# Kernel tuning notes

Measured on AMD Instinct MI355X. Metric: run time of the kernel, lower is better.

## Reference

```python
import jax, jax.numpy as jnp
import numpy as np

N_NODES = 100000


def gcn_conv(x, edge_index, W, b):
    """PyG-style GCNConv: x' = D^-1/2 (A+I) D^-1/2 (x W) + b (self-loops added)."""
    n = x.shape[0]
    h = x @ W  # [N, out]
    loop = jnp.arange(n, dtype=edge_index.dtype)
    src = jnp.concatenate([edge_index[0], loop])  # [E+N]
    dst = jnp.concatenate([edge_index[1], loop])
    deg = jax.ops.segment_sum(jnp.ones_like(dst, dtype=h.dtype), dst, num_segments=n)
    dinv = jnp.where(deg > 0, jax.lax.rsqrt(deg), 0.0)
    norm = dinv[src] * dinv[dst]  # [E+N]
    # gather -> scale -> scatter-add aggregation
    out = jax.ops.segment_sum(norm[:, None] * h[src], dst, num_segments=n)
    return out + b


def setup_inputs() -> dict:
    key = jax.random.key(0)
    k1, k2, k3, k4 = jax.random.split(key, 4)
    n, e = N_NODES, 2560000
    x = jax.random.normal(k1, (n, 2), dtype=jnp.float32)
    edge_index = jax.random.randint(k2, (2, e), 0, n, dtype=jnp.int32)
    hidden = 32
    W1 = jax.random.normal(k3, (2, hidden), dtype=jnp.float32) * (1.0 / np.sqrt(2))
    b1 = jnp.zeros((hidden,), dtype=jnp.float32)
    W2 = jax.random.normal(k4, (hidden, 1), dtype=jnp.float32) * (1.0 / np.sqrt(hidden))
    b2 = jnp.zeros((1,), dtype=jnp.float32)
    return {"x": x, "edge_index": edge_index, "W1": W1, "b1": b1, "W2": W2, "b2": b2}


def reference(x, edge_index, W1, b1, W2, b2):
    h = jax.nn.relu(gcn_conv(x, edge_index, W1, b1))
    return gcn_conv(h, edge_index, W2, b2)  # [N, 1]
```

## Files before the change

### kernel.cpp

```cpp
#include <hip/hip_runtime.h>


#define NRMAX 32
#define AGG_BLKS 16
#define CHUNK 4096
#define NCHMAX 1024
#define DBITS 12
#define DMASK 4095


__global__ void k_px(const float2* __restrict__ x, const int* __restrict__ pdeg,
                     float* __restrict__ dinv, float2* __restrict__ px, int n) {
    int i = blockIdx.x * blockDim.x + threadIdx.x;
    if (i >= n) return;
    int deg = 1;
#pragma unroll
    for (int b = 0; b < AGG_BLKS; ++b) deg += pdeg[b * n + i];
    float d = rsqrtf((float)deg);
    dinv[i] = d;
    float2 xv = x[i];
    px[i] = make_float2(d * xv.x, d * xv.y);
}

__global__ void k_node(const float2* __restrict__ px, const float2* __restrict__ pP,
                       const float* __restrict__ dinv,
                       const float* __restrict__ W1, const float* __restrict__ b1,
                       const float* __restrict__ W2, float* __restrict__ s, int n) {
    int i = blockIdx.x * blockDim.x + threadIdx.x;
    if (i >= n) return;
    float2 v = px[i];
    float ax = v.x, ay = v.y;
#pragma unroll
    for (int b = 0; b < AGG_BLKS; ++b) {
        float2 p = pP[b * n + i];
        ax += p.x; ay += p.y;
    }
    float d = dinv[i];
    float dot = 0.f;
#pragma unroll
    for (int j = 0; j < 32; ++j) {
        float acc = fmaf(ax, W1[j], ay * W1[32 + j]);
        float h = fmaxf(fmaf(d, acc, b1[j]), 0.f);
        dot = fmaf(h, W2[j], dot);
    }
    s[i] = d * dot;
}

__global__ void k_out(const float* __restrict__ s, const float* __restrict__ ps,
                      const float* __restrict__ dinv, const float* __restrict__ b2,
                      float* __restrict__ out, int n) {
    int i = blockIdx.x * blockDim.x + threadIdx.x;
    if (i >= n) return;
    float acc = s[i];
#pragma unroll
    for (int b = 0; b < AGG_BLKS; ++b) acc += ps[b * n + i];
    out[i] = dinv[i] * acc + b2[0];
}


__global__ void k_cnt(const int* __restrict__ dst, int* __restrict__ cnt,
                      int e, int NR) {
    __shared__ int h[NRMAX];
    if (threadIdx.x < NRMAX) h[threadIdx.x] = 0;
    __syncthreads();
    int c0 = blockIdx.x * CHUNK;
    int c1 = min(c0 + CHUNK, e);
    int len = c1 - c0, lq = len >> 2;
    const int4* d4 = (const int4*)(dst + c0);
    for (int j = threadIdx.x; j < lq; j += blockDim.x) {
        int4 v = d4[j];
        atomicAdd(&h[v.x >> DBITS], 1);
        atomicAdd(&h[v.y >> DBITS], 1);
        atomicAdd(&h[v.z >> DBITS], 1);
        atomicAdd(&h[v.w >> DBITS], 1);
    }
    if (threadIdx.x == 0)
        for (int i = lq * 4; i < len; ++i) atomicAdd(&h[dst[c0 + i] >> DBITS], 1);
    __syncthreads();
    if (threadIdx.x < NR) cnt[(threadIdx.x << 10) + blockIdx.x] = h[threadIdx.x];
}

__global__ __launch_bounds__(1024)
void k_scan(const int* __restrict__ cnt, int* __restrict__ ofs,
            int* __restrict__ bstart, int* __restrict__ bcnt, int NR, int NCH) {
    __shared__ int tot[NRMAX], bs[NRMAX];
    int tid = threadIdx.x, lane = tid & 63, wid = tid >> 6;
    for (int r = wid; r < NR; r += 16) {
        int base = 0;
        for (int c0 = 0; c0 < NCH; c0 += 64) {
            int c = c0 + lane;
            int orig = (c < NCH) ? cnt[(r << 10) + c] : 0;
            int v = orig;
#pragma unroll
            for (int d = 1; d < 64; d <<= 1) {
                int u = __shfl_up(v, d);
                if (lane >= d) v += u;
            }
            if (c < NCH) ofs[(r << 10) + c] = base + v - orig;
            base += __shfl(v, 63);
        }
        tot[r] = base;
    }
    __syncthreads();
    if (tid == 0) {
        int acc = 0;
        for (int r = 0; r < NR; ++r) {
            bs[r] = acc; bstart[r] = acc; bcnt[r] = tot[r];
            acc += (tot[r] + 3) & ~3;
        }
    }
    __syncthreads();
    for (int i = tid; i < (NR << 10); i += 1024) {
        int c = i & (NCHMAX - 1);
        if (c < NCH) ofs[i] += bs[i >> 10];
    }
}

__global__ void k_bscatter(const int* __restrict__ src, const int* __restrict__ dst,
                           const int* __restrict__ ofs, unsigned* __restrict__ packed,
                           int e, int NR) {
    __shared__ int h[NRMAX], lofs[NRMAX], cur[NRMAX], gbase[NRMAX];
    __shared__ unsigned sbuf[CHUNK];
    int blk = blockIdx.x;
    int c0 = blk * CHUNK;
    int c1 = min(c0 + CHUNK, e);
    int len = c1 - c0, lq = len >> 2;
    if (threadIdx.x < NRMAX) h[threadIdx.x] = 0;
    __syncthreads();
    const int4* d4 = (const int4*)(dst + c0);
    const int4* s4 = (const int4*)(src + c0);
    for (int j = threadIdx.x; j < lq; j += blockDim.x) {
        int4 v = d4[j];
        atomicAdd(&h[v.x >> DBITS], 1);
        atomicAdd(&h[v.y >> DBITS], 1);
        atomicAdd(&h[v.z >> DBITS], 1);
        atomicAdd(&h[v.w >> DBITS], 1);
    }
    if (threadIdx.x == 0)
        for (int i = lq * 4; i < len; ++i) atomicAdd(&h[dst[c0 + i] >> DBITS], 1);
    __syncthreads();
    if (threadIdx.x == 0) {
        int acc = 0;
        for (int r = 0; r < NR; ++r) { lofs[r] = acc; acc += h[r]; }
    }
    __syncthreads();
    if (threadIdx.x < NR) {
        cur[threadIdx.x]   = lofs[threadIdx.x];
        gbase[threadIdx.x] = ofs[(threadIdx.x << 10) + blk];
    }
    __syncthreads();
    for (int j = threadIdx.x; j < lq; j += blockDim.x) {
        int4 dv = d4[j];
        int4 sv = s4[j];
        int r0 = dv.x >> DBITS; int t0 = atomicAdd(&cur[r0], 1);
        sbuf[t0] = ((unsigned)sv.x << DBITS) | (unsigned)(dv.x & DMASK);
        int r1 = dv.y >> DBITS; int t1 = atomicAdd(&cur[r1], 1);
        sbuf[t1] = ((unsigned)sv.y << DBITS) | (unsigned)(dv.y & DMASK);
        int r2 = dv.z >> DBITS; int t2 = atomicAdd(&cur[r2], 1);
        sbuf[t2] = ((unsigned)sv.z << DBITS) | (unsigned)(dv.z & DMASK);
        int r3 = dv.w >> DBITS; int t3 = atomicAdd(&cur[r3], 1);
        sbuf[t3] = ((unsigned)sv.w << DBITS) | (unsigned)(dv.w & DMASK);
    }
    if (threadIdx.x == 0)
        for (int i = lq * 4; i < len; ++i) {
            int d = dst[c0 + i];
            int r = d >> DBITS;
            int t = atomicAdd(&cur[r], 1);
            sbuf[t] = ((unsigned)src[c0 + i] << DBITS) | (unsigned)(d & DMASK);
        }
    __syncthreads();
    for (int r = 0; r < NR; ++r) {
        int c = h[r], lo = lofs[r], gb = gbase[r];
        for (int t = threadIdx.x; t < c; t += blockDim.x)
            packed[gb + t] = sbuf[lo + t];
    }
}


__global__ __launch_bounds__(1024, 8)
void k_deg(const unsigned* __restrict__ packed, const int* __restrict__ bstart,
           const int* __restrict__ bcnt, int* __restrict__ pdeg, int n) {
    __shared__ int acc[DMASK + 1];
    int r = blockIdx.y, b = blockIdx.x;
    int rs_r = min(DMASK + 1, n - (r << DBITS));
    for (int t = threadIdx.x; t < rs_r; t += blockDim.x) acc[t] = 0;
    __syncthreads();
    int c = bcnt[r], base = bstart[r];
    int q = (c + 3) >> 2;
    int qper = (q + AGG_BLKS - 1) / AGG_BLKS;
    int qlo = b * qper, qhi = min(qlo + qper, q);
    const uint4* p4 = (const uint4*)(packed + base);
    for (int j = qlo + threadIdx.x; j < qhi; j += blockDim.x) {
        uint4 v = p4[j];
        int lim = c - j * 4;
        atomicAdd(&acc[v.x & DMASK], 1);
        if (lim > 1) atomicAdd(&acc[v.y & DMASK], 1);
        if (lim > 2) atomicAdd(&acc[v.z & DMASK], 1);
        if (lim > 3) atomicAdd(&acc[v.w & DMASK], 1);
    }
    __syncthreads();
    int nb = b * n + (r << DBITS);
    for (int t = threadIdx.x; t < rs_r; t += blockDim.x) pdeg[nb + t] = acc[t];
}

__global__ __launch_bounds__(1024, 8)
void k_agg1(const unsigned* __restrict__ packed, const int* __restrict__ bstart,
            const int* __restrict__ bcnt, const float2* __restrict__ px,
            float2* __restrict__ pP, int n) {
    __shared__ float acc[2 * (DMASK + 1)];
    int r = blockIdx.y, b = blockIdx.x;
    int rs_r = min(DMASK + 1, n - (r << DBITS));
    for (int t = threadIdx.x; t < 2 * rs_r; t += blockDim.x) acc[t] = 0.f;
    __syncthreads();
    int c = bcnt[r], base = bstart[r];
    int q = (c + 3) >> 2;
    int qper = (q + AGG_BLKS - 1) / AGG_BLKS;
    int qlo = b * qper, qhi = min(qlo + qper, q);
    const uint4* p4 = (const uint4*)(packed + base);
    int nm1 = n - 1;
    for (int j = qlo + threadIdx.x; j < qhi; j += blockDim.x) {
        uint4 v = p4[j];
        int i0 = (int)(v.x >> DBITS);
        int i1 = min((int)(v.y >> DBITS), nm1);
        int i2 = min((int)(v.z >> DBITS), nm1);
        int i3 = min((int)(v.w >> DBITS), nm1);
        float2 g0 = px[i0], g1 = px[i1], g2 = px[i2], g3 = px[i3];
        int lim = c - j * 4;
        int d0 = (v.x & DMASK) * 2;
        atomicAdd(&acc[d0], g0.x); atomicAdd(&acc[d0 + 1], g0.y);
        if (lim > 1) { int d1 = (v.y & DMASK) * 2; atomicAdd(&acc[d1], g1.x); atomicAdd(&acc[d1 + 1], g1.y); }
        if (lim > 2) { int d2 = (v.z & DMASK) * 2; atomicAdd(&acc[d2], g2.x); atomicAdd(&acc[d2 + 1], g2.y); }
        if (lim > 3) { int d3 = (v.w & DMASK) * 2; atomicAdd(&acc[d3], g3.x); atomicAdd(&acc[d3 + 1], g3.y); }
    }
    __syncthreads();
    int nb = b * n + (r << DBITS);
    for (int t = threadIdx.x; t < rs_r; t += blockDim.x)
        pP[nb + t] = make_float2(acc[2 * t], acc[2 * t + 1]);
}

__global__ __launch_bounds__(1024, 8)
void k_agg2(const unsigned* __restrict__ packed, const int* __restrict__ bstart,
            const int* __restrict__ bcnt, const float* __restrict__ s,
            float* __restrict__ ps, int n) {
    __shared__ float acc[DMASK + 1];
    int r = blockIdx.y, b = blockIdx.x;
    int rs_r = min(DMASK + 1, n - (r << DBITS));
    for (int t = threadIdx.x; t < rs_r; t += blockDim.x) acc[t] = 0.f;
    __syncthreads();
    int c = bcnt[r], base = bstart[r];
    int q = (c + 3) >> 2;
    int qper = (q + AGG_BLKS - 1) / AGG_BLKS;
    int qlo = b * qper, qhi = min(qlo + qper, q);
    const uint4* p4 = (const uint4*)(packed + base);
    int nm1 = n - 1;
    for (int j = qlo + threadIdx.x; j < qhi; j += blockDim.x) {
        uint4 v = p4[j];
        int i0 = (int)(v.x >> DBITS);
        int i1 = min((int)(v.y >> DBITS), nm1);
        int i2 = min((int)(v.z >> DBITS), nm1);
        int i3 = min((int)(v.w >> DBITS), nm1);
        float g0 = s[i0], g1 = s[i1], g2 = s[i2], g3 = s[i3];
        int lim = c - j * 4;
        atomicAdd(&acc[v.x & DMASK], g0);
        if (lim > 1) atomicAdd(&acc[v.y & DMASK], g1);
        if (lim > 2) atomicAdd(&acc[v.z & DMASK], g2);
        if (lim > 3) atomicAdd(&acc[v.w & DMASK], g3);
    }
    __syncthreads();
    int nb = b * n + (r << DBITS);
    for (int t = threadIdx.x; t < rs_r; t += blockDim.x) ps[nb + t] = acc[t];
}


__global__ void f_zero(int* __restrict__ ideg, float2* __restrict__ P, int n) {
    int i = blockIdx.x * blockDim.x + threadIdx.x;
    if (i < n) { ideg[i] = 0; P[i] = make_float2(0.f, 0.f); }
}
__global__ void f_count(const int* __restrict__ dst, int* __restrict__ ideg, int e) {
    int i = blockIdx.x * blockDim.x + threadIdx.x;
    if (i < e) atomicAdd(&ideg[dst[i]], 1);
}
__global__ void f_px(const float2* __restrict__ x, const int* __restrict__ ideg,
                     float* __restrict__ dinv, float2* __restrict__ px, int n) {
    int i = blockIdx.x * blockDim.x + threadIdx.x;
    if (i >= n) return;
    float d = rsqrtf((float)(1 + ideg[i]));
    dinv[i] = d;
    float2 xv = x[i];
    px[i] = make_float2(d * xv.x, d * xv.y);
}
__global__ void f_scatter_px(const int* __restrict__ src, const int* __restrict__ dst,
                             const float2* __restrict__ px, float* __restrict__ Pf, int e) {
    int i = blockIdx.x * blockDim.x + threadIdx.x;
    if (i >= e) return;
    int sidx = src[i], d = dst[i];
    float2 v = px[sidx];
    atomicAdd(&Pf[2 * d], v.x);
    atomicAdd(&Pf[2 * d + 1], v.y);
}
__global__ void f_node(const float2* __restrict__ px, const float2* __restrict__ P,
                       const float* __restrict__ dinv,
                       const float* __restrict__ W1, const float* __restrict__ b1,
                       const float* __restrict__ W2,
                       float* __restrict__ s, float* __restrict__ S, int n) {
    int i = blockIdx.x * blockDim.x + threadIdx.x;
    if (i >= n) return;
    float d = dinv[i];
    float2 v = px[i], p = P[i];
    float ax = v.x + p.x, ay = v.y + p.y;
    float dot = 0.f;
#pragma unroll
    for (int j = 0; j < 32; ++j) {
        float acc = fmaf(ax, W1[j], ay * W1[32 + j]);
        float h = fmaxf(fmaf(d, acc, b1[j]), 0.f);
        dot = fmaf(h, W2[j], dot);
    }
    float sv = d * dot;
    s[i] = sv;
    S[i] = sv;
}
__global__ void f_scatter_s(const int* __restrict__ src, const int* __restrict__ dst,
                            const float* __restrict__ s, float* __restrict__ S, int e) {
    int i = blockIdx.x * blockDim.x + threadIdx.x;
    if (i < e) atomicAdd(&S[dst[i]], s[src[i]]);
}
__global__ void f_out(const float* __restrict__ S, const float* __restrict__ dinv,
                      const float* __restrict__ b2, float* __restrict__ out, int n) {
    int i = blockIdx.x * blockDim.x + threadIdx.x;
    if (i < n) out[i] = dinv[i] * S[i] + b2[0];
}


extern "C" void kernel_launch(void* const* d_in, const int* in_sizes, int n_in,
                              void* d_out, int out_size, void* d_ws, size_t ws_size,
                              hipStream_t stream) {
    const float* x  = (const float*)d_in[0];
    const int*   ei = (const int*)d_in[1];
    const float* W1 = (const float*)d_in[2];
    const float* b1 = (const float*)d_in[3];
    const float* W2 = (const float*)d_in[4];
    const float* b2 = (const float*)d_in[5];
    float* out = (float*)d_out;

    int n = in_sizes[0] / 2;
    int e = in_sizes[1] / 2;
    const int* src = ei;
    const int* dst = ei + e;
    int NR  = (n + DMASK) >> DBITS;
    int NCH = (e + CHUNK - 1) / CHUNK;

    char* ws = (char*)d_ws;
    auto align = [](size_t v) { return (v + 255) & ~(size_t)255; };
    size_t off = 0;
    float*  dinv = (float*) (ws + off); off = align(off + (size_t)n * 4);
    float2* px   = (float2*)(ws + off); off = align(off + (size_t)n * 8);
    float*  s    = (float*) (ws + off); off = align(off + (size_t)n * 4);
    int*    pdeg = (int*)   (ws + off); off = align(off + (size_t)AGG_BLKS * n * 4);
    float2* pP   = (float2*)(ws + off); off = align(off + (size_t)AGG_BLKS * n * 8);
    float*  ps   = (float*) (ws + off); off = align(off + (size_t)AGG_BLKS * n * 4);
    int*    bstart = (int*)(ws + off); off = align(off + NRMAX * 4);
    int*    bcnt   = (int*)(ws + off); off = align(off + NRMAX * 4);
    int*    cnt    = (int*)(ws + off); off = align(off + (size_t)NRMAX * NCHMAX * 4);
    int*    ofs    = (int*)(ws + off); off = align(off + (size_t)NRMAX * NCHMAX * 4);
    unsigned* packed = (unsigned*)(ws + off);
    size_t need = off + (size_t)(e + 4 * NRMAX) * 4;

    const int B = 256;
    int gn = (n + B - 1) / B, ge = (e + B - 1) / B;

    bool fast = (need <= ws_size) && (NR <= NRMAX) && (NCH <= NCHMAX) && (n <= (1 << 17));

    if (fast) {
        dim3 ag(AGG_BLKS, NR);
        k_cnt     <<<NCH, B, 0, stream>>>(dst, cnt, e, NR);
        k_scan    <<<1, 1024, 0, stream>>>(cnt, ofs, bstart, bcnt, NR, NCH);
        k_bscatter<<<NCH, B, 0, stream>>>(src, dst, ofs, packed, e, NR);
        k_deg     <<<ag, 1024, 0, stream>>>(packed, bstart, bcnt, pdeg, n);
        k_px      <<<gn, B, 0, stream>>>((const float2*)x, pdeg, dinv, px, n);
        k_agg1    <<<ag, 1024, 0, stream>>>(packed, bstart, bcnt, px, pP, n);
        k_node    <<<gn, B, 0, stream>>>(px, pP, dinv, W1, b1, W2, s, n);
        k_agg2    <<<ag, 1024, 0, stream>>>(packed, bstart, bcnt, s, ps, n);
        k_out     <<<gn, B, 0, stream>>>(s, ps, dinv, b2, out, n);
    } else {
        int*   ideg = pdeg;
        float2* P   = pP;
        float* S    = ps;
        f_zero      <<<gn, B, 0, stream>>>(ideg, P, n);
        f_count     <<<ge, B, 0, stream>>>(dst, ideg, e);
        f_px        <<<gn, B, 0, stream>>>((const float2*)x, ideg, dinv, px, n);
        f_scatter_px<<<ge, B, 0, stream>>>(src, dst, px, (float*)P, e);
        f_node      <<<gn, B, 0, stream>>>(px, P, dinv, W1, b1, W2, s, S, n);
        f_scatter_s <<<ge, B, 0, stream>>>(src, dst, s, S, e);
        f_out       <<<gn, B, 0, stream>>>(S, dinv, b2, out, n);
    }
}
```

Measured before the change: 117.6 us.

## Bin edges by destination and source block for gather locality in aggregation

Edges are now bucketed into 2D bins keyed by destination block and source block, not by destination block alone. Within each destination bucket they are therefore sorted by source block, so the px and s gathers in the aggregation kernels touch a narrow source range and cache better. Each bin is padded to a multiple of four with a sentinel value, and the scatter writes each edge directly to a precomputed destination. AGG_BLKS also drops from 16 to 8, which halves the partial-sum arrays that later kernels reduce. In exchange, the count and scatter kernels use larger shared histograms and write out many more, smaller segments.

```diff
diff --git a/kernel.cpp b/kernel.cpp
--- a/kernel.cpp
+++ b/kernel.cpp
@@ -1,12 +1,14 @@
 #include <hip/hip_runtime.h>
 
 
+#define NBMAX 1024
 #define NRMAX 32
-#define AGG_BLKS 16
+#define AGG_BLKS 8
 #define CHUNK 4096
-#define NCHMAX 1024
+#define NCHP 640
 #define DBITS 12
 #define DMASK 4095
+#define NOEDGE 0xFFFFFFFFu
 
 
 __global__ void k_px(const float2* __restrict__ x, const int* __restrict__ pdeg,
@@ -58,145 +60,165 @@
 }
 
 
-__global__ void k_cnt(const int* __restrict__ dst, int* __restrict__ cnt,
-                      int e, int NR) {
-    __shared__ int h[NRMAX];
-    if (threadIdx.x < NRMAX) h[threadIdx.x] = 0;
-    __syncthreads();
-    int c0 = blockIdx.x * CHUNK;
-    int c1 = min(c0 + CHUNK, e);
+__global__ void k_cnt(const int* __restrict__ src, const int* __restrict__ dst,
+                      int* __restrict__ cnt, int e, int NS, int NB) {
+    __shared__ int h[NBMAX];
+    for (int t = threadIdx.x; t < NB; t += blockDim.x) h[t] = 0;
+    __syncthreads();
+    int c0 = blockIdx.x * CHUNK, c1 = min(c0 + CHUNK, e);
     int len = c1 - c0, lq = len >> 2;
     const int4* d4 = (const int4*)(dst + c0);
+    const int4* s4 = (const int4*)(src + c0);
     for (int j = threadIdx.x; j < lq; j += blockDim.x) {
-        int4 v = d4[j];
-        atomicAdd(&h[v.x >> DBITS], 1);
-        atomicAdd(&h[v.y >> DBITS], 1);
-        atomicAdd(&h[v.z >> DBITS], 1);
-        atomicAdd(&h[v.w >> DBITS], 1);
+        int4 dv = d4[j], sv = s4[j];
+        atomicAdd(&h[(dv.x >> DBITS) * NS + (sv.x >> DBITS)], 1);
+        atomicAdd(&h[(dv.y >> DBITS) * NS + (sv.y >> DBITS)], 1);
+        atomicAdd(&h[(dv.z >> DBITS) * NS + (sv.z >> DBITS)], 1);
+        atomicAdd(&h[(dv.w >> DBITS) * NS + (sv.w >> DBITS)], 1);
     }
     if (threadIdx.x == 0)
-        for (int i = lq * 4; i < len; ++i) atomicAdd(&h[dst[c0 + i] >> DBITS], 1);
-    __syncthreads();
-    if (threadIdx.x < NR) cnt[(threadIdx.x << 10) + blockIdx.x] = h[threadIdx.x];
+        for (int i = lq * 4; i < len; ++i)
+            atomicAdd(&h[(dst[c0 + i] >> DBITS) * NS + (src[c0 + i] >> DBITS)], 1);
+    __syncthreads();
+    for (int t = threadIdx.x; t < NB; t += blockDim.x)
+        cnt[t * NCHP + blockIdx.x] = h[t];
 }
 
 __global__ __launch_bounds__(1024)
 void k_scan(const int* __restrict__ cnt, int* __restrict__ ofs,
-            int* __restrict__ bstart, int* __restrict__ bcnt, int NR, int NCH) {
-    __shared__ int tot[NRMAX], bs[NRMAX];
-    int tid = threadIdx.x, lane = tid & 63, wid = tid >> 6;
-    for (int r = wid; r < NR; r += 16) {
+            int* __restrict__ gbin, int* __restrict__ rbase, int* __restrict__ rlenp,
+            unsigned* __restrict__ packed, int NB, int NS, int NCH) {
+    __shared__ int tot[NBMAX], gb[NBMAX];
+    int tid = threadIdx.x, lane = tid & 63, w = tid >> 6;
+    for (int bin = w; bin < NB; bin += 16) {
         int base = 0;
         for (int c0 = 0; c0 < NCH; c0 += 64) {
             int c = c0 + lane;
-            int orig = (c < NCH) ? cnt[(r << 10) + c] : 0;
+            int orig = (c < NCH) ? cnt[bin * NCHP + c] : 0;
             int v = orig;
 #pragma unroll
             for (int d = 1; d < 64; d <<= 1) {
                 int u = __shfl_up(v, d);
                 if (lane >= d) v += u;
             }
-            if (c < NCH) ofs[(r << 10) + c] = base + v - orig;
+            if (c < NCH) ofs[bin * NCHP + c] = base + v - orig;
             base += __shfl(v, 63);
         }
-        tot[r] = base;
+        tot[bin] = base;
     }
     __syncthreads();
     if (tid == 0) {
         int acc = 0;
-        for (int r = 0; r < NR; ++r) {
-            bs[r] = acc; bstart[r] = acc; bcnt[r] = tot[r];
-            acc += (tot[r] + 3) & ~3;
-        }
-    }
-    __syncthreads();
-    for (int i = tid; i < (NR << 10); i += 1024) {
-        int c = i & (NCHMAX - 1);
-        if (c < NCH) ofs[i] += bs[i >> 10];
-    }
-}
-
-__global__ void k_bscatter(const int* __restrict__ src, const int* __restrict__ dst,
-                           const int* __restrict__ ofs, unsigned* __restrict__ packed,
-                           int e, int NR) {
-    __shared__ int h[NRMAX], lofs[NRMAX], cur[NRMAX], gbase[NRMAX];
+        for (int bin = 0; bin < NB; ++bin) { gb[bin] = acc; acc += (tot[bin] + 3) & ~3; }
+        int NR_ = NB / NS;
+        for (int r = 0; r < NR_; ++r) {
+            int b0 = gb[r * NS];
+            int b1 = (r + 1 < NR_) ? gb[(r + 1) * NS] : acc;
+            rbase[r] = b0; rlenp[r] = b1 - b0;
+        }
+    }
+    __syncthreads();
+    for (int bin = tid; bin < NB; bin += 1024) {
+        gbin[bin] = gb[bin];
+        int t = tot[bin], p = (t + 3) & ~3;
+        for (int k = t; k < p; ++k) packed[gb[bin] + k] = NOEDGE;
+    }
+}
+
+__global__ __launch_bounds__(256)
+void k_bscatter(const int* __restrict__ src, const int* __restrict__ dst,
+                const int* __restrict__ ofs, const int* __restrict__ gbin,
+                unsigned* __restrict__ packed, int e, int NS, int NB) {
+    __shared__ int h[NBMAX], lofs[NBMAX], curx[NBMAX], gb[NBMAX];
     __shared__ unsigned sbuf[CHUNK];
+    __shared__ int dest[CHUNK];
     int blk = blockIdx.x;
-    int c0 = blk * CHUNK;
-    int c1 = min(c0 + CHUNK, e);
+    int c0 = blk * CHUNK, c1 = min(c0 + CHUNK, e);
     int len = c1 - c0, lq = len >> 2;
-    if (threadIdx.x < NRMAX) h[threadIdx.x] = 0;
+    for (int t = threadIdx.x; t < NB; t += blockDim.x) h[t] = 0;
     __syncthreads();
     const int4* d4 = (const int4*)(dst + c0);
     const int4* s4 = (const int4*)(src + c0);
     for (int j = threadIdx.x; j < lq; j += blockDim.x) {
-        int4 v = d4[j];
-        atomicAdd(&h[v.x >> DBITS], 1);
-        atomicAdd(&h[v.y >> DBITS], 1);
-        atomicAdd(&h[v.z >> DBITS], 1);
-        atomicAdd(&h[v.w >> DBITS], 1);
+        int4 dv = d4[j], sv = s4[j];
+        atomicAdd(&h[(dv.x >> DBITS) * NS + (sv.x >> DBITS)], 1);
+        atomicAdd(&h[(dv.y >> DBITS) * NS + (sv.y >> DBITS)], 1);
+        atomicAdd(&h[(dv.z >> DBITS) * NS + (sv.z >> DBITS)], 1);
+        atomicAdd(&h[(dv.w >> DBITS) * NS + (sv.w >> DBITS)], 1);
     }
     if (threadIdx.x == 0)
-        for (int i = lq * 4; i < len; ++i) atomicAdd(&h[dst[c0 + i] >> DBITS], 1);
+        for (int i = lq * 4; i < len; ++i)
+            atomicAdd(&h[(dst[c0 + i] >> DBITS) * NS + (src[c0 + i] >> DBITS)], 1);
     __syncthreads();
     if (threadIdx.x == 0) {
         int acc = 0;
-        for (int r = 0; r < NR; ++r) { lofs[r] = acc; acc += h[r]; }
-    }
-    __syncthreads();
-    if (threadIdx.x < NR) {
-        cur[threadIdx.x]   = lofs[threadIdx.x];
-        gbase[threadIdx.x] = ofs[(threadIdx.x << 10) + blk];
+        for (int b = 0; b < NB; ++b) { lofs[b] = acc; acc += h[b]; }
+    }
+    __syncthreads();
+    for (int t = threadIdx.x; t < NB; t += blockDim.x) {
+        curx[t] = lofs[t];
+        gb[t] = gbin[t] + ofs[t * NCHP + blk];
     }
     __syncthreads();
     for (int j = threadIdx.x; j < lq; j += blockDim.x) {
-        int4 dv = d4[j];
-        int4 sv = s4[j];
-        int r0 = dv.x >> DBITS; int t0 = atomicAdd(&cur[r0], 1);
-        sbuf[t0] = ((unsigned)sv.x << DBITS) | (unsigned)(dv.x & DMASK);
-        int r1 = dv.y >> DBITS; int t1 = atomicAdd(&cur[r1], 1);
-        sbuf[t1] = ((unsigned)sv.y << DBITS) | (unsigned)(dv.y & DMASK);
-        int r2 = dv.z >> DBITS; int t2 = atomicAdd(&cur[r2], 1);
-        sbuf[t2] = ((unsigned)sv.z << DBITS) | (unsigned)(dv.z & DMASK);
-        int r3 = dv.w >> DBITS; int t3 = atomicAdd(&cur[r3], 1);
-        sbuf[t3] = ((unsigned)sv.w << DBITS) | (unsigned)(dv.w & DMASK);
+        int4 dv = d4[j], sv = s4[j];
+        {
+            int b = (dv.x >> DBITS) * NS + (sv.x >> DBITS);
+            int sl = atomicAdd(&curx[b], 1);
+            sbuf[sl] = ((unsigned)sv.x << DBITS) | (unsigned)(dv.x & DMASK);
+            dest[sl] = gb[b] + (sl - lofs[b]);
+        }
+        {
+            int b = (dv.y >> DBITS) * NS + (sv.y >> DBITS);
+            int sl = atomicAdd(&curx[b], 1);
+            sbuf[sl] = ((unsigned)sv.y << DBITS) | (unsigned)(dv.y & DMASK);
+            dest[sl] = gb[b] + (sl - lofs[b]);
+        }
+        {
+            int b = (dv.z >> DBITS) * NS + (sv.z >> DBITS);
+            int sl = atomicAdd(&curx[b], 1);
+            sbuf[sl] = ((unsigned)sv.z << DBITS) | (unsigned)(dv.z & DMASK);
+            dest[sl] = gb[b] + (sl - lofs[b]);
+        }
+        {
+            int b = (dv.w >> DBITS) * NS + (sv.w >> DBITS);
+            int sl = atomicAdd(&curx[b], 1);
+            sbuf[sl] = ((unsigned)sv.w << DBITS) | (unsigned)(dv.w & DMASK);
+            dest[sl] = gb[b] + (sl - lofs[b]);
+        }
     }
     if (threadIdx.x == 0)
         for (int i = lq * 4; i < len; ++i) {
-            int d = dst[c0 + i];
-            int r = d >> DBITS;
-            int t = atomicAdd(&cur[r], 1);
-            sbuf[t] = ((unsigned)src[c0 + i] << DBITS) | (unsigned)(d & DMASK);
-        }
-    __syncthreads();
-    for (int r = 0; r < NR; ++r) {
-        int c = h[r], lo = lofs[r], gb = gbase[r];
-        for (int t = threadIdx.x; t < c; t += blockDim.x)
-            packed[gb + t] = sbuf[lo + t];
-    }
+            int d = dst[c0 + i], sx = src[c0 + i];
+            int b = (d >> DBITS) * NS + (sx >> DBITS);
+            int sl = atomicAdd(&curx[b], 1);
+            sbuf[sl] = ((unsigned)sx << DBITS) | (unsigned)(d & DMASK);
+            dest[sl] = gb[b] + (sl - lofs[b]);
+        }
+    __syncthreads();
+    for (int t = threadIdx.x; t < len; t += blockDim.x)
+        packed[dest[t]] = sbuf[t];
 }
 
 
 __global__ __launch_bounds__(1024, 8)
-void k_deg(const unsigned* __restrict__ packed, const int* __restrict__ bstart,
-           const int* __restrict__ bcnt, int* __restrict__ pdeg, int n) {
+void k_deg(const unsigned* __restrict__ packed, const int* __restrict__ rbase,
+           const int* __restrict__ rlenp, int* __restrict__ pdeg, int n) {
     __shared__ int acc[DMASK + 1];
     int r = blockIdx.y, b = blockIdx.x;
     int rs_r = min(DMASK + 1, n - (r << DBITS));
     for (int t = threadIdx.x; t < rs_r; t += blockDim.x) acc[t] = 0;
     __syncthreads();
-    int c = bcnt[r], base = bstart[r];
-    int q = (c + 3) >> 2;
+    int base = rbase[r], q = rlenp[r] >> 2;
     int qper = (q + AGG_BLKS - 1) / AGG_BLKS;
     int qlo = b * qper, qhi = min(qlo + qper, q);
     const uint4* p4 = (const uint4*)(packed + base);
     for (int j = qlo + threadIdx.x; j < qhi; j += blockDim.x) {
         uint4 v = p4[j];
-        int lim = c - j * 4;
-        atomicAdd(&acc[v.x & DMASK], 1);
-        if (lim > 1) atomicAdd(&acc[v.y & DMASK], 1);
-        if (lim > 2) atomicAdd(&acc[v.z & DMASK], 1);
-        if (lim > 3) atomicAdd(&acc[v.w & DMASK], 1);
+        if (v.x != NOEDGE) atomicAdd(&acc[v.x & DMASK], 1);
+        if (v.y != NOEDGE) atomicAdd(&acc[v.y & DMASK], 1);
+        if (v.z != NOEDGE) atomicAdd(&acc[v.z & DMASK], 1);
+        if (v.w != NOEDGE) atomicAdd(&acc[v.w & DMASK], 1);
     }
     __syncthreads();
     int nb = b * n + (r << DBITS);
@@ -204,33 +226,30 @@
 }
 
 __global__ __launch_bounds__(1024, 8)
-void k_agg1(const unsigned* __restrict__ packed, const int* __restrict__ bstart,
-            const int* __restrict__ bcnt, const float2* __restrict__ px,
+void k_agg1(const unsigned* __restrict__ packed, const int* __restrict__ rbase,
+            const int* __restrict__ rlenp, const float2* __restrict__ px,
             float2* __restrict__ pP, int n) {
     __shared__ float acc[2 * (DMASK + 1)];
     int r = blockIdx.y, b = blockIdx.x;
     int rs_r = min(DMASK + 1, n - (r << DBITS));
     for (int t = threadIdx.x; t < 2 * rs_r; t += blockDim.x) acc[t] = 0.f;
     __syncthreads();
-    int c = bcnt[r], base = bstart[r];
-    int q = (c + 3) >> 2;
+    int base = rbase[r], q = rlenp[r] >> 2;
     int qper = (q + AGG_BLKS - 1) / AGG_BLKS;
     int qlo = b * qper, qhi = min(qlo + qper, q);
     const uint4* p4 = (const uint4*)(packed + base);
     int nm1 = n - 1;
     for (int j = qlo + threadIdx.x; j < qhi; j += blockDim.x) {
         uint4 v = p4[j];
-        int i0 = (int)(v.x >> DBITS);
+        int i0 = min((int)(v.x >> DBITS), nm1);
         int i1 = min((int)(v.y >> DBITS), nm1);
         int i2 = min((int)(v.z >> DBITS), nm1);
         int i3 = min((int)(v.w >> DBITS), nm1);
         float2 g0 = px[i0], g1 = px[i1], g2 = px[i2], g3 = px[i3];
-        int lim = c - j * 4;
-        int d0 = (v.x & DMASK) * 2;
-        atomicAdd(&acc[d0], g0.x); atomicAdd(&acc[d0 + 1], g0.y);
-        if (lim > 1) { int d1 = (v.y & DMASK) * 2; atomicAdd(&acc[d1], g1.x); atomicAdd(&acc[d1 + 1], g1.y); }
-        if (lim > 2) { int d2 = (v.z & DMASK) * 2; atomicAdd(&acc[d2], g2.x); atomicAdd(&acc[d2 + 1], g2.y); }
-        if (lim > 3) { int d3 = (v.w & DMASK) * 2; atomicAdd(&acc[d3], g3.x); atomicAdd(&acc[d3 + 1], g3.y); }
+        if (v.x != NOEDGE) { int d0 = (v.x & DMASK) * 2; atomicAdd(&acc[d0], g0.x); atomicAdd(&acc[d0 + 1], g0.y); }
+        if (v.y != NOEDGE) { int d1 = (v.y & DMASK) * 2; atomicAdd(&acc[d1], g1.x); atomicAdd(&acc[d1 + 1], g1.y); }
+        if (v.z != NOEDGE) { int d2 = (v.z & DMASK) * 2; atomicAdd(&acc[d2], g2.x); atomicAdd(&acc[d2 + 1], g2.y); }
+        if (v.w != NOEDGE) { int d3 = (v.w & DMASK) * 2; atomicAdd(&acc[d3], g3.x); atomicAdd(&acc[d3 + 1], g3.y); }
     }
     __syncthreads();
     int nb = b * n + (r << DBITS);
@@ -239,32 +258,30 @@
 }
 
 __global__ __launch_bounds__(1024, 8)
-void k_agg2(const unsigned* __restrict__ packed, const int* __restrict__ bstart,
-            const int* __restrict__ bcnt, const float* __restrict__ s,
+void k_agg2(const unsigned* __restrict__ packed, const int* __restrict__ rbase,
+            const int* __restrict__ rlenp, const float* __restrict__ s,
             float* __restrict__ ps, int n) {
     __shared__ float acc[DMASK + 1];
     int r = blockIdx.y, b = blockIdx.x;
     int rs_r = min(DMASK + 1, n - (r << DBITS));
     for (int t = threadIdx.x; t < rs_r; t += blockDim.x) acc[t] = 0.f;
     __syncthreads();
-    int c = bcnt[r], base = bstart[r];
-    int q = (c + 3) >> 2;
+    int base = rbase[r], q = rlenp[r] >> 2;
     int qper = (q + AGG_BLKS - 1) / AGG_BLKS;
     int qlo = b * qper, qhi = min(qlo + qper, q);
     const uint4* p4 = (const uint4*)(packed + base);
     int nm1 = n - 1;
     for (int j = qlo + threadIdx.x; j < qhi; j += blockDim.x) {
         uint4 v = p4[j];
-        int i0 = (int)(v.x >> DBITS);
+        int i0 = min((int)(v.x >> DBITS), nm1);
         int i1 = min((int)(v.y >> DBITS), nm1);
         int i2 = min((int)(v.z >> DBITS), nm1);
         int i3 = min((int)(v.w >> DBITS), nm1);
         float g0 = s[i0], g1 = s[i1], g2 = s[i2], g3 = s[i3];
-        int lim = c - j * 4;
-        atomicAdd(&acc[v.x & DMASK], g0);
-        if (lim > 1) atomicAdd(&acc[v.y & DMASK], g1);
-        if (lim > 2) atomicAdd(&acc[v.z & DMASK], g2);
-        if (lim > 3) atomicAdd(&acc[v.w & DMASK], g3);
+        if (v.x != NOEDGE) atomicAdd(&acc[v.x & DMASK], g0);
+        if (v.y != NOEDGE) atomicAdd(&acc[v.y & DMASK], g1);
+        if (v.z != NOEDGE) atomicAdd(&acc[v.z & DMASK], g2);
+        if (v.w != NOEDGE) atomicAdd(&acc[v.w & DMASK], g3);
     }
     __syncthreads();
     int nb = b * n + (r << DBITS);
@@ -347,6 +364,8 @@
     const int* src = ei;
     const int* dst = ei + e;
     int NR  = (n + DMASK) >> DBITS;
+    int NS  = NR;
+    int NB  = NR * NS;
     int NCH = (e + CHUNK - 1) / CHUNK;
 
     char* ws = (char*)d_ws;
@@ -358,28 +377,29 @@
     int*    pdeg = (int*)   (ws + off); off = align(off + (size_t)AGG_BLKS * n * 4);
     float2* pP   = (float2*)(ws + off); off = align(off + (size_t)AGG_BLKS * n * 8);
     float*  ps   = (float*) (ws + off); off = align(off + (size_t)AGG_BLKS * n * 4);
-    int*    bstart = (int*)(ws + off); off = align(off + NRMAX * 4);
-    int*    bcnt   = (int*)(ws + off); off = align(off + NRMAX * 4);
-    int*    cnt    = (int*)(ws + off); off = align(off + (size_t)NRMAX * NCHMAX * 4);
-    int*    ofs    = (int*)(ws + off); off = align(off + (size_t)NRMAX * NCHMAX * 4);
+    int*    rbase = (int*)(ws + off); off = align(off + NRMAX * 4);
+    int*    rlenp = (int*)(ws + off); off = align(off + NRMAX * 4);
+    int*    gbin  = (int*)(ws + off); off = align(off + NBMAX * 4);
+    int*    cnt   = (int*)(ws + off); off = align(off + (size_t)NBMAX * NCHP * 4);
+    int*    ofs   = (int*)(ws + off); off = align(off + (size_t)NBMAX * NCHP * 4);
     unsigned* packed = (unsigned*)(ws + off);
-    size_t need = off + (size_t)(e + 4 * NRMAX) * 4;
+    size_t need = off + (size_t)(e + 4 * NBMAX) * 4;
 
     const int B = 256;
     int gn = (n + B - 1) / B, ge = (e + B - 1) / B;
 
-    bool fast = (need <= ws_size) && (NR <= NRMAX) && (NCH <= NCHMAX) && (n <= (1 << 17));
+    bool fast = (need <= ws_size) && (NB <= NBMAX) && (NCH <= NCHP) && (NR <= NRMAX);
 
     if (fast) {
         dim3 ag(AGG_BLKS, NR);
-        k_cnt     <<<NCH, B, 0, stream>>>(dst, cnt, e, NR);
-        k_scan    <<<1, 1024, 0, stream>>>(cnt, ofs, bstart, bcnt, NR, NCH);
-        k_bscatter<<<NCH, B, 0, stream>>>(src, dst, ofs, packed, e, NR);
-        k_deg     <<<ag, 1024, 0, stream>>>(packed, bstart, bcnt, pdeg, n);
+        k_cnt     <<<NCH, B, 0, stream>>>(src, dst, cnt, e, NS, NB);
+        k_scan    <<<1, 1024, 0, stream>>>(cnt, ofs, gbin, rbase, rlenp, packed, NB, NS, NCH);
+        k_bscatter<<<NCH, B, 0, stream>>>(src, dst, ofs, gbin, packed, e, NS, NB);
+        k_deg     <<<ag, 1024, 0, stream>>>(packed, rbase, rlenp, pdeg, n);
         k_px      <<<gn, B, 0, stream>>>((const float2*)x, pdeg, dinv, px, n);
-        k_agg1    <<<ag, 1024, 0, stream>>>(packed, bstart, bcnt, px, pP, n);
+        k_agg1    <<<ag, 1024, 0, stream>>>(packed, rbase, rlenp, px, pP, n);
         k_node    <<<gn, B, 0, stream>>>(px, pP, dinv, W1, b1, W2, s, n);
-        k_agg2    <<<ag, 1024, 0, stream>>>(packed, bstart, bcnt, s, ps, n);
+        k_agg2    <<<ag, 1024, 0, stream>>>(packed, rbase, rlenp, s, ps, n);
         k_out     <<<gn, B, 0, stream>>>(s, ps, dinv, b2, out, n);
     } else {
         int*   ideg = pdeg;
```

Result: slower. 336.3 us (+186.1%).
